# Kernel optimization log

Hardware: AMD Instinct MI355X
Metric: run time of the kernel (lower is better)

## Reference

```python
import jax, jax.numpy as jnp
import numpy as np
from itertools import combinations

DILATIONS = [1, 2, 4, 8]
NUM_KERNELS = 84  # C(9,3)
KERNEL_LEN = 9


def setup_inputs() -> dict:
    key = jax.random.key(0)
    k_x, k_mask, k_bias, k_mean, k_std = jax.random.split(key, 5)
    B, L, C = 64, 2048, 8
    D = len(DILATIONS)
    F = 4  # features (biases) per kernel per dilation
    num_features = D * NUM_KERNELS * F

    # MiniRocket fixed kernels: -1 everywhere, +2 at each 3-index combination
    idx = np.asarray(list(combinations(range(KERNEL_LEN), 3)), dtype=np.int64)
    base = np.full((NUM_KERNELS, KERNEL_LEN), -1.0, dtype=np.float32)
    for i in range(NUM_KERNELS):
        base[i, idx[i]] = 2.0

    x = jax.random.normal(k_x, (B, L, C), dtype=jnp.float32)
    # binary channel masks per (dilation, kernel): which channels contribute
    channel_masks = (jax.random.uniform(k_mask, (D, NUM_KERNELS, C)) < 0.5).astype(jnp.float32)
    bias_matrices = jax.random.normal(k_bias, (D, NUM_KERNELS, F), dtype=jnp.float32)
    feature_mean = jax.random.normal(k_mean, (num_features,), dtype=jnp.float32)
    feature_std = jax.random.uniform(k_std, (num_features,), minval=0.5, maxval=1.5, dtype=jnp.float32)
    return {
        "x": x,
        "kernels": jnp.asarray(base),
        "channel_masks": channel_masks,
        "bias_matrices": bias_matrices,
        "feature_mean": feature_mean,
        "feature_std": feature_std,
    }


def _extract(x, kernels, channel_masks, bias_matrices):
    B, L, C = x.shape
    D, K, F = bias_matrices.shape
    x_cf = jnp.transpose(x, (0, 2, 1))  # [B, C, L]
    dtype = x.dtype
    t = jnp.arange(L)
    feats_all = []
    for d_idx, dil in enumerate(DILATIONS):
        pad = (KERNEL_LEN - 1) * dil // 2  # = 4*dil, so conv output length == L
        # Since the depthwise kernel is identical across channels for a given
        # kernel index, masked-channel-sum commutes with the conv:
        # response[b,k,:] = conv(sum_c mask[k,c] * x[b,c,:], kernel_k)
        mixed = jnp.einsum('kc,bcl->bkl', channel_masks[d_idx], x_cf)  # [B,K,L]
        resp = jax.lax.conv_general_dilated(
            mixed, kernels[:, None, :],
            window_strides=(1,), padding=[(pad, pad)],
            rhs_dilation=(dil,),
            dimension_numbers=('NCH', 'OIH', 'NCH'),
            feature_group_count=K,
        )  # [B, K, L]
        # PPV time-weights: kernels with odd (dilation_index + kernel_index)
        # are trimmed to the interior [pad, L-pad); others use the full length.
        should_trim = (pad > 0) and (L - 2 * pad > 0)
        interior = ((t >= pad) & (t < L - pad)).astype(dtype)  # [L]
        w_full = jnp.full((L,), 1.0 / L, dtype=dtype)
        w_trim = interior / jnp.asarray(L - 2 * pad, dtype=dtype)
        parity_odd = ((d_idx + jnp.arange(K)) % 2 == 1) & should_trim  # [K]
        w = jnp.where(parity_odd[:, None], w_trim[None, :], w_full[None, :])  # [K,L]
        # PPV: fraction of timesteps where response exceeds each bias
        ind = (resp[:, :, None, :] > bias_matrices[d_idx][None, :, :, None]).astype(dtype)  # [B,K,F,L]
        feats = jnp.einsum('bkfl,kl->bkf', ind, w)  # [B,K,F]
        feats_all.append(feats.reshape(B, K * F))
    return jnp.concatenate(feats_all, axis=1)  # [B, D*K*F]


def reference(x, kernels, channel_masks, bias_matrices, feature_mean, feature_std):
    flat = _extract(x, kernels, channel_masks, bias_matrices)
    return (flat - feature_mean) / feature_std
```

## Files before the change

kernel.cpp:

```cpp
#include <hip/hip_runtime.h>

#define TL 2048
#define TC 8
#define TK 84
#define TF 4
#define TD 4
#define ROWS 352
#define NFEAT (TD * TK * TF)
#define KF (TK * TF)
#define NQ 8

typedef unsigned int u32;
typedef __fp16 hf8 __attribute__((ext_vector_type(8)));
typedef float f32x4 __attribute__((ext_vector_type(4)));

__device__ __forceinline__ u32 pkrtz(float a, float b) {
    return __builtin_bit_cast(u32, __builtin_amdgcn_cvt_pkrtz(a, b));
}
__device__ __forceinline__ int swzrow(int e) { return e ^ ((e >> 3) & 7); }

__device__ __forceinline__ u32 red16(u32 v) {
    v += (u32)__builtin_amdgcn_update_dpp(0, (int)v, 0xB1,  0xF, 0xF, true);
    v += (u32)__builtin_amdgcn_update_dpp(0, (int)v, 0x4E,  0xF, 0xF, true);
    v += (u32)__builtin_amdgcn_update_dpp(0, (int)v, 0x141, 0xF, 0xF, true);
    v += (u32)__builtin_amdgcn_update_dpp(0, (int)v, 0x140, 0xF, 0xF, true);
    return v;
}

__global__ __launch_bounds__(256, 4) void mr_main(
    const float* __restrict__ x,
    const float* __restrict__ kern,
    const float* __restrict__ cmask,
    const float* __restrict__ bias,
    int* __restrict__ ws)
{
    __shared__ __align__(16) uint4 xh[ROWS];
    __shared__ __align__(16) uint4 Alds[1152];
    __shared__ __align__(16) float4 blds[TK];
    __shared__ u32 feats2[6][4][16];

    const int bx = blockIdx.x;
    const int q = bx & 7, d = (bx >> 3) & 3, b = bx >> 5;
    const int tid = threadIdx.x, lane = tid & 63, w = tid >> 6;
    const int dil = 1 << d, pad = 4 << d;
    const int t0 = q * 256;
    const float* xb = x + (size_t)b * TL * TC;

    if (tid < TK) blds[tid] = *(const float4*)(bias + ((size_t)d * TK + tid) * TF);

    for (int f = tid; f < 1152; f += 256) {
        const int col = f & 15, lg = (f >> 4) & 3, kbkt = f >> 6;
        const int kt = kbkt / 3, kb = kbkt % 3;
        const int k = kt * 16 + col, j = kb * 4 + lg;
        uint4 v = {0u, 0u, 0u, 0u};
        if (k < TK && j < 9) {
            const float wv = kern[k * 9 + j];
            const float* mp = cmask + ((size_t)d * TK + k) * TC;
            const float4 m0 = *(const float4*)mp;
            const float4 m1 = *(const float4*)(mp + 4);
            v.x = pkrtz(m0.x != 0.f ? wv : 0.f, m0.y != 0.f ? wv : 0.f);
            v.y = pkrtz(m0.z != 0.f ? wv : 0.f, m0.w != 0.f ? wv : 0.f);
            v.z = pkrtz(m1.x != 0.f ? wv : 0.f, m1.y != 0.f ? wv : 0.f);
            v.w = pkrtz(m1.z != 0.f ? wv : 0.f, m1.w != 0.f ? wv : 0.f);
        }
        Alds[f] = v;
    }

    for (int e = tid; e < ROWS; e += 256) {
        const int pos = t0 - 32 + e;
        uint4 v = {0u, 0u, 0u, 0u};
        if (pos >= 0 && pos < TL) {
            const float4* xp = (const float4*)(xb + (size_t)pos * TC);
            const float4 a = xp[0], h = xp[1];
            v.x = pkrtz(a.x, a.y); v.y = pkrtz(a.z, a.w);
            v.z = pkrtz(h.x, h.y); v.w = pkrtz(h.z, h.w);
        }
        xh[swzrow(e)] = v;
    }
    __syncthreads();

    const int col = lane & 15, lg = lane >> 4;

    hf8 bf[12];
    #pragma unroll
    for (int i = 0; i < 4; ++i)
        #pragma unroll
        for (int kb = 0; kb < 3; ++kb) {
            const int e = 32 + col - 4 * dil + (w * 4 + i) * 16 + (kb * 4 + lg) * dil;
            bf[i * 3 + kb] = __builtin_bit_cast(hf8, xh[swzrow(e)]);
        }

    bool interior[4];
    #pragma unroll
    for (int i = 0; i < 4; ++i) {
        const int tfirst = t0 + (w * 4 + i) * 16;
        interior[i] = (tfirst >= pad) && (tfirst + 16 <= TL - pad);
    }

    hf8 af0 = __builtin_bit_cast(hf8, Alds[0 * 64 + lane]);
    hf8 af1 = __builtin_bit_cast(hf8, Alds[1 * 64 + lane]);
    hf8 af2 = __builtin_bit_cast(hf8, Alds[2 * 64 + lane]);

    for (int kt = 0; kt < 6; ++kt) {
        hf8 an0, an1, an2;
        if (kt < 5) {
            an0 = __builtin_bit_cast(hf8, Alds[((kt + 1) * 3 + 0) * 64 + lane]);
            an1 = __builtin_bit_cast(hf8, Alds[((kt + 1) * 3 + 1) * 64 + lane]);
            an2 = __builtin_bit_cast(hf8, Alds[((kt + 1) * 3 + 2) * 64 + lane]);
        }

        float4 bq[4];
        #pragma unroll
        for (int rg = 0; rg < 4; ++rg) {
            int k = kt * 16 + lg * 4 + rg;
            k = (k < TK) ? k : (TK - 1);
            bq[rg] = blds[k];
        }

        u32 cnt[4] = {0u, 0u, 0u, 0u};

        #pragma unroll
        for (int i = 0; i < 4; ++i) {
            f32x4 C = {0.f, 0.f, 0.f, 0.f};
            C = __builtin_amdgcn_mfma_f32_16x16x32_f16(af0, bf[i * 3 + 0], C, 0, 0, 0);
            C = __builtin_amdgcn_mfma_f32_16x16x32_f16(af1, bf[i * 3 + 1], C, 0, 0, 0);
            C = __builtin_amdgcn_mfma_f32_16x16x32_f16(af2, bf[i * 3 + 2], C, 0, 0, 0);

            if (interior[i]) {
                #pragma unroll
                for (int rg = 0; rg < 4; ++rg) {
                    const float cv = C[rg];
                    cnt[rg] += (cv > bq[rg].x) ? 0x1u : 0u;
                    cnt[rg] += (cv > bq[rg].y) ? 0x100u : 0u;
                    cnt[rg] += (cv > bq[rg].z) ? 0x10000u : 0u;
                    cnt[rg] += (cv > bq[rg].w) ? 0x1000000u : 0u;
                }
            } else {
                const int t = t0 + (w * 4 + i) * 16 + col;
                const bool ok = (t >= pad && t < TL - pad);
                #pragma unroll
                for (int rg = 0; rg < 4; ++rg) {
                    const float cv = C[rg];
                    const bool use = ((d ^ rg) & 1) ? ok : true;
                    cnt[rg] += (use && cv > bq[rg].x) ? 0x1u : 0u;
                    cnt[rg] += (use && cv > bq[rg].y) ? 0x100u : 0u;
                    cnt[rg] += (use && cv > bq[rg].z) ? 0x10000u : 0u;
                    cnt[rg] += (use && cv > bq[rg].w) ? 0x1000000u : 0u;
                }
            }
        }

        #pragma unroll
        for (int rg = 0; rg < 4; ++rg) cnt[rg] = red16(cnt[rg]);

        if (col == 0) {
            #pragma unroll
            for (int rg = 0; rg < 4; ++rg)
                feats2[kt][w][lg * 4 + rg] = cnt[rg];
        }

        if (kt < 5) { af0 = an0; af1 = an1; af2 = an2; }
    }

    __syncthreads();
    for (int idx = tid; idx < KF; idx += 256) {
        const int k = idx >> 2, f = idx & 3;
        const int kt = k >> 4, r = k & 15;
        int cnt = 0;
        #pragma unroll
        for (int wv = 0; wv < 4; ++wv)
            cnt += (int)((feats2[kt][wv][r] >> (8 * f)) & 0xFFu);
        ws[(size_t)bx * KF + idx] = cnt;
    }
}

__global__ void mr_fin(const int* __restrict__ ws, const float* __restrict__ fmean,
                       const float* __restrict__ fstd, float* __restrict__ out) {
    const int o = blockIdx.x * 256 + threadIdx.x;
    const int fid = o % NFEAT, b = o / NFEAT;
    const int d = fid / KF, idx = fid % KF, k = idx >> 2;
    const int base = ((b * 32 + d * 8) * KF) + idx;
    int cnt = 0;
    #pragma unroll
    for (int q = 0; q < NQ; ++q) cnt += ws[base + q * KF];
    const float denom = ((d + k) & 1) ? (float)(TL - (8 << d)) : (float)TL;
    out[o] = ((float)cnt / denom - fmean[fid]) / fstd[fid];
}

extern "C" void kernel_launch(void* const* d_in, const int* in_sizes, int n_in,
                              void* d_out, int out_size, void* d_ws, size_t ws_size,
                              hipStream_t stream) {
    const float* x     = (const float*)d_in[0];
    const float* kern  = (const float*)d_in[1];
    const float* cmask = (const float*)d_in[2];
    const float* bias  = (const float*)d_in[3];
    const float* fmean = (const float*)d_in[4];
    const float* fstd  = (const float*)d_in[5];
    float* out = (float*)d_out;
    int* ws = (int*)d_ws;

    hipLaunchKernelGGL(mr_main, dim3(64 * TD * NQ), dim3(256), 0, stream,
                       x, kern, cmask, bias, ws);
    hipLaunchKernelGGL(mr_fin, dim3(64 * NFEAT / 256), dim3(256), 0, stream,
                       ws, fmean, fstd, out);
}
```

Measured before the change: 33.41 us.

## Precompute fp16 packed input and MFMA A-fragments in separate prep kernels

Adds two prep kernels. One converts x to padded fp16 rows once per batch, and the other builds the masked kernel A-fragments once per dilation. The main kernel then copies these from global memory into LDS instead of recomputing them in each of the 2048 blocks. This removes redundant conversion and mask work, which was repeated 32x per batch row and 512x per dilation. The cost is two extra kernel launches and an extra round trip through global memory for the converted data.

```diff
diff --git a/kernel.cpp b/kernel.cpp
--- a/kernel.cpp
+++ b/kernel.cpp
@@ -5,7 +5,8 @@
 #define TK 84
 #define TF 4
 #define TD 4
-#define ROWS 352
+#define ROWS 384
+#define PXR 2208
 #define NFEAT (TD * TK * TF)
 #define KF (TK * TF)
 #define NQ 8
@@ -27,10 +28,45 @@
     return v;
 }
 
+__global__ void mr_prepx(const float* __restrict__ x, uint4* __restrict__ xg) {
+    const int idx = blockIdx.x * 256 + threadIdx.x;
+    if (idx >= 64 * PXR) return;
+    const int b = idx / PXR, pos = (idx % PXR) - 32;
+    uint4 v = {0u, 0u, 0u, 0u};
+    if (pos >= 0 && pos < TL) {
+        const float4* xp = (const float4*)(x + ((size_t)b * TL + pos) * TC);
+        const float4 a = xp[0], h = xp[1];
+        v.x = pkrtz(a.x, a.y); v.y = pkrtz(a.z, a.w);
+        v.z = pkrtz(h.x, h.y); v.w = pkrtz(h.z, h.w);
+    }
+    xg[idx] = v;
+}
+
+__global__ void mr_prepa(const float* __restrict__ kern, const float* __restrict__ cmask,
+                         uint4* __restrict__ A) {
+    const int idx = blockIdx.x * 256 + threadIdx.x;
+    if (idx >= TD * 18 * 64) return;
+    const int lane = idx & 63, kbkt = (idx >> 6) % 18, d = idx / (18 * 64);
+    const int kt = kbkt / 3, kb = kbkt % 3;
+    const int col = lane & 15, lg = lane >> 4;
+    const int k = kt * 16 + col, j = kb * 4 + lg;
+    uint4 v = {0u, 0u, 0u, 0u};
+    if (k < TK && j < 9) {
+        const float wv = kern[k * 9 + j];
+        const float* mp = cmask + ((size_t)d * TK + k) * TC;
+        const float4 m0 = *(const float4*)mp;
+        const float4 m1 = *(const float4*)(mp + 4);
+        v.x = pkrtz(m0.x != 0.f ? wv : 0.f, m0.y != 0.f ? wv : 0.f);
+        v.y = pkrtz(m0.z != 0.f ? wv : 0.f, m0.w != 0.f ? wv : 0.f);
+        v.z = pkrtz(m1.x != 0.f ? wv : 0.f, m1.y != 0.f ? wv : 0.f);
+        v.w = pkrtz(m1.z != 0.f ? wv : 0.f, m1.w != 0.f ? wv : 0.f);
+    }
+    A[idx] = v;
+}
+
 __global__ __launch_bounds__(256, 4) void mr_main(
-    const float* __restrict__ x,
-    const float* __restrict__ kern,
-    const float* __restrict__ cmask,
+    const uint4* __restrict__ xg,
+    const uint4* __restrict__ Ag,
     const float* __restrict__ bias,
     int* __restrict__ ws)
 {
@@ -44,39 +80,14 @@
     const int tid = threadIdx.x, lane = tid & 63, w = tid >> 6;
     const int dil = 1 << d, pad = 4 << d;
     const int t0 = q * 256;
-    const float* xb = x + (size_t)b * TL * TC;
 
     if (tid < TK) blds[tid] = *(const float4*)(bias + ((size_t)d * TK + tid) * TF);
 
-    for (int f = tid; f < 1152; f += 256) {
-        const int col = f & 15, lg = (f >> 4) & 3, kbkt = f >> 6;
-        const int kt = kbkt / 3, kb = kbkt % 3;
-        const int k = kt * 16 + col, j = kb * 4 + lg;
-        uint4 v = {0u, 0u, 0u, 0u};
-        if (k < TK && j < 9) {
-            const float wv = kern[k * 9 + j];
-            const float* mp = cmask + ((size_t)d * TK + k) * TC;
-            const float4 m0 = *(const float4*)mp;
-            const float4 m1 = *(const float4*)(mp + 4);
-            v.x = pkrtz(m0.x != 0.f ? wv : 0.f, m0.y != 0.f ? wv : 0.f);
-            v.y = pkrtz(m0.z != 0.f ? wv : 0.f, m0.w != 0.f ? wv : 0.f);
-            v.z = pkrtz(m1.x != 0.f ? wv : 0.f, m1.y != 0.f ? wv : 0.f);
-            v.w = pkrtz(m1.z != 0.f ? wv : 0.f, m1.w != 0.f ? wv : 0.f);
-        }
-        Alds[f] = v;
-    }
-
-    for (int e = tid; e < ROWS; e += 256) {
-        const int pos = t0 - 32 + e;
-        uint4 v = {0u, 0u, 0u, 0u};
-        if (pos >= 0 && pos < TL) {
-            const float4* xp = (const float4*)(xb + (size_t)pos * TC);
-            const float4 a = xp[0], h = xp[1];
-            v.x = pkrtz(a.x, a.y); v.y = pkrtz(a.z, a.w);
-            v.z = pkrtz(h.x, h.y); v.w = pkrtz(h.z, h.w);
-        }
-        xh[swzrow(e)] = v;
-    }
+    const uint4* Ad = Ag + d * 1152;
+    for (int f = tid; f < 1152; f += 256) Alds[f] = Ad[f];
+
+    const uint4* xw = xg + (size_t)b * PXR + t0;
+    for (int e = tid; e < ROWS; e += 256) xh[swzrow(e)] = xw[e];
     __syncthreads();
 
     const int col = lane & 15, lg = lane >> 4;
@@ -197,10 +208,17 @@
     const float* fmean = (const float*)d_in[4];
     const float* fstd  = (const float*)d_in[5];
     float* out = (float*)d_out;
-    int* ws = (int*)d_ws;
-
+
+    uint4* xgws = (uint4*)d_ws;
+    uint4* Aws  = (uint4*)((char*)d_ws + 64 * PXR * 16);
+    int*   cws  = (int*)((char*)d_ws + 64 * PXR * 16 + TD * 18 * 64 * 16);
+
+    hipLaunchKernelGGL(mr_prepx, dim3((64 * PXR + 255) / 256), dim3(256), 0, stream,
+                       x, xgws);
+    hipLaunchKernelGGL(mr_prepa, dim3((TD * 18 * 64 + 255) / 256), dim3(256), 0, stream,
+                       kern, cmask, Aws);
     hipLaunchKernelGGL(mr_main, dim3(64 * TD * NQ), dim3(256), 0, stream,
-                       x, kern, cmask, bias, ws);
+                       xgws, Aws, bias, cws);
     hipLaunchKernelGGL(mr_fin, dim3(64 * NFEAT / 256), dim3(256), 0, stream,
-                       ws, fmean, fstd, out);
-}
+                       cws, fmean, fstd, out);
+}
```

New measurement: 38.36 us. +14.8%, slower.
